# Kernel optimization log

Hardware: AMD Instinct MI355X
Metric: run time of the kernel (lower is better)

Reference implementation:

```python
import jax, jax.numpy as jnp
import numpy as np
from jax import lax

KS = 3            # kernel_size
K = 32            # cluster_num
NB = 32           # num_base_kernels
HID = 64          # mlp_hidden_dim
COUT = 64         # out_channels
MAX_ITER = 20
TOL = 0.005


def _unfold3(x):
    # torch nn.Unfold(k=3, pad=1): output channel order is (c, kh, kw)
    b, c, h, w = x.shape
    xp = jnp.pad(x, ((0, 0), (0, 0), (1, 1), (1, 1)))
    cols = [xp[:, :, i:i + h, j:j + w] for i in range(KS) for j in range(KS)]
    p = jnp.stack(cols, axis=2)  # [B, C, 9, H, W]
    return p.reshape(b, c * KS * KS, h * w).transpose(0, 2, 1)  # [B, HW, C*9]


def _kmeans_single(key, sample):
    # sample: [N, D]. Lloyd iterations with early stop on total center shift.
    n, d = sample.shape
    centers0 = sample[jax.random.permutation(key, n)[:K]]

    def assign(centers):
        d2 = (jnp.sum(sample * sample, 1, keepdims=True)
              - 2.0 * (sample @ centers.T)
              + jnp.sum(centers * centers, 1))
        return jnp.argmin(d2, axis=1)

    def body(carry):
        i, centers, _ = carry
        a = assign(centers)
        oh = jax.nn.one_hot(a, K, dtype=sample.dtype)  # [N, K]
        counts = oh.sum(0)                             # [K]
        sums = oh.T @ sample                           # [K, D]
        new = jnp.where(counts[:, None] > 0,
                        sums / jnp.maximum(counts, 1.0)[:, None],
                        centers)
        shift = jnp.sum(jnp.linalg.norm(new - centers, axis=1))
        return (i + 1, new, shift)

    def cond(carry):
        i, _, shift = carry
        return jnp.logical_and(i < MAX_ITER, shift >= TOL * n)

    init = (jnp.int32(0), centers0, jnp.asarray(jnp.inf, sample.dtype))
    _, centers, _ = lax.while_loop(cond, body, init)
    return assign(centers)


def _kmeans(features):
    keys = jax.random.split(jax.random.key(42), features.shape[0])
    return jax.vmap(_kmeans_single)(keys, features)


def _mlp(x, w1, b1, w2, b2, w3, b3):
    h = jax.nn.relu(x @ w1 + b1)
    h = jax.nn.relu(h @ w2 + b2)
    return h @ w3 + b3


def setup_inputs() -> dict:
    key = jax.random.key(0)
    ks = jax.random.split(key, 16)
    B, C, H, W = 2, 32, 64, 64
    F = C * KS * KS
    fan = 1.0 / np.sqrt(F)
    fanh = 1.0 / np.sqrt(HID)
    return {
        'x': jax.random.normal(ks[0], (B, C, H, W), jnp.float32),
        'base_kernels': jax.random.normal(ks[1], (NB, F, COUT), jnp.float32) * np.sqrt(2.0 / F),
        'kg_w1': jax.random.normal(ks[2], (F, HID), jnp.float32) * fan,
        'kg_b1': jnp.zeros((HID,), jnp.float32),
        'kg_w2': jax.random.normal(ks[3], (HID, HID), jnp.float32) * fanh,
        'kg_b2': jnp.zeros((HID,), jnp.float32),
        'kg_w3': jax.random.normal(ks[4], (HID, NB), jnp.float32) * fanh,
        'kg_b3': jnp.zeros((NB,), jnp.float32),
        'bg_w1': jax.random.normal(ks[5], (F, HID), jnp.float32) * fan,
        'bg_b1': jnp.zeros((HID,), jnp.float32),
        'bg_w2': jax.random.normal(ks[6], (HID, HID), jnp.float32) * fanh,
        'bg_b2': jnp.zeros((HID,), jnp.float32),
        'bg_w3': jax.random.normal(ks[7], (HID, COUT), jnp.float32) * fanh,
        'bg_b3': jnp.zeros((COUT,), jnp.float32),
    }


def reference(x, base_kernels, kg_w1, kg_b1, kg_w2, kg_b2, kg_w3, kg_b3,
              bg_w1, bg_b1, bg_w2, bg_b2, bg_w3, bg_b3):
    B, C, H, W = x.shape
    patches = _unfold3(x)  # [B, P, F] with F = C*9
    P = patches.shape[1]
    # observation features: mean over kernel area per channel
    obs = patches.reshape(B, P, C, KS * KS).mean(-1)  # [B, P, C]
    idx = _kmeans(obs)  # [B, P] int cluster assignments

    # per-cluster centers of the full patch features (scatter-mean)
    oh = jax.nn.one_hot(idx, K, dtype=patches.dtype)          # [B, P, K]
    sums = jnp.einsum('bpk,bpf->bkf', oh, patches)            # [B, K, F]
    counts = jnp.maximum(oh.sum(1), 1.0)                      # [B, K]
    centers = sums / counts[:, :, None]                       # [B, K, F]

    # adaptive kernels = softmax-mixture of base kernels
    attn = jax.nn.softmax(_mlp(centers, kg_w1, kg_b1, kg_w2, kg_b2, kg_w3, kg_b3), axis=-1)  # [B,K,NB]
    kernels = jnp.einsum('bkn,nfc->bkfc', attn, base_kernels)  # [B, K, F, COUT]
    biases = _mlp(centers, bg_w1, bg_b1, bg_w2, bg_b2, bg_w3, bg_b3)  # [B, K, COUT]

    # combine: out[b,p] = patches[b,p] @ kernels[b, idx[b,p]] + biases[b, idx[b,p]]
    bidx = jnp.arange(B)[:, None]
    wtok = kernels[bidx, idx]   # [B, P, F, COUT]
    btok = biases[bidx, idx]    # [B, P, COUT]
    out = jnp.einsum('bpf,bpfc->bpc', patches, wtok) + btok
    out = out.transpose(0, 2, 1).reshape(B, COUT, H, W)
    return (out, idx)
```

## Files before the change

kernel.cpp:

```cpp
#include <hip/hip_runtime.h>
#include <hip/hip_bf16.h>
#include <vector>
#include <algorithm>
#include <utility>
#include <stdint.h>

#define BB 2
#define PP 4096
#define FF 288
#define KK 32
#define NBASE 32
#define HID 64
#define COUT 64
#define NWG_KM 32
#define SUBS 16
#define OUT_ELEMS 524288

#define THREEFRY_PARTITIONABLE 1

typedef unsigned short u16;

#define OFF_IDX    512
#define OFF_ATTN   33280
#define OFF_BIAS   41472
#define OFF_PART   57856
#define OFF_CNTS   320000
#define OFF_CPART  328192
#define OFF_WG     1544704
#define OFF_BAR2   3904000

struct InitIdx { int v[2][32]; };

__device__ __forceinline__ float bf2f(u16 u){
  union { unsigned int i; float f; } cv; cv.i = ((unsigned int)u) << 16; return cv.f;
}
__device__ __forceinline__ u16 f2bf(float f){
  union { float f; unsigned int i; } cv; cv.f = f;
  unsigned int x = cv.i;
  unsigned int r = (x + 0x7FFFu + ((x >> 16) & 1u)) >> 16;
  return (u16)r;
}
__device__ __forceinline__ float u_lo(unsigned int u){
  union { unsigned int i; float f; } cv; cv.i = u << 16; return cv.f;
}
__device__ __forceinline__ float u_hi(unsigned int u){
  union { unsigned int i; float f; } cv; cv.i = u & 0xFFFF0000u; return cv.f;
}

__device__ __forceinline__ void st_agent(float* p, float v){
  __hip_atomic_store(reinterpret_cast<unsigned int*>(p), __float_as_uint(v),
                     __ATOMIC_RELAXED, __HIP_MEMORY_SCOPE_AGENT);
}
__device__ __forceinline__ float ld_agent(const float* p){
  unsigned int u = __hip_atomic_load(reinterpret_cast<const unsigned int*>(p),
                                     __ATOMIC_RELAXED, __HIP_MEMORY_SCOPE_AGENT);
  return __uint_as_float(u);
}

template<bool BF>
__device__ __forceinline__ float ld(const void* p, size_t i){
  if constexpr (BF) { return bf2f(((const u16*)p)[i]); }
  else              { return ((const float*)p)[i]; }
}
template<bool BF>
__device__ __forceinline__ void st(void* p, size_t i, float v){
  if constexpr (BF) { ((u16*)p)[i] = f2bf(v); }
  else              { ((float*)p)[i] = v; }
}

template<bool BF>
__device__ __forceinline__ float obs_chan(const void* x, size_t bi, int h, int w){
  float s = 0.f;
  #pragma unroll
  for (int dh=-1; dh<=1; ++dh){
    int hh = h + dh;
    #pragma unroll
    for (int dw=-1; dw<=1; ++dw){
      int ww = w + dw;
      float v = 0.f;
      if ((unsigned)hh < 64u && (unsigned)ww < 64u) v = ld<BF>(x, bi + (hh<<6) + ww);
      s += v;
    }
  }
  return s / 9.0f;
}

__device__ __forceinline__ void gbar16(int* slots, int mb, int sub, int epoch){
  asm volatile("s_waitcnt vmcnt(0)" ::: "memory");
  __syncthreads();
  const int t = threadIdx.x;
  if (t == 0)
    __hip_atomic_store(&slots[(mb*16 + sub)*16], epoch, __ATOMIC_RELAXED, __HIP_MEMORY_SCOPE_AGENT);
  if (t < 16){
    while (__hip_atomic_load(&slots[(mb*16 + t)*16], __ATOMIC_RELAXED, __HIP_MEMORY_SCOPE_AGENT) < epoch){}
  }
  __atomic_signal_fence(__ATOMIC_SEQ_CST);
  __syncthreads();
}

__global__ __launch_bounds__(256) void kDetect(const void* __restrict__ x, int* flag,
                                               int* slots){
  __shared__ int cnt;
  if (threadIdx.x == 0) cnt = 0;
  for (int i = threadIdx.x; i < 512; i += 256) slots[i] = 0;
  __syncthreads();
  const u16* p = (const u16*)x;
  int bad = 0;
  for (int i = threadIdx.x; i < 1024; i += 256){
    u16 u = p[2*i];
    unsigned e = (u >> 7) & 0xFFu;
    if (e >= 131u) ++bad;
  }
  atomicAdd(&cnt, bad);
  __syncthreads();
  if (threadIdx.x == 0) *flag = (cnt < 102) ? 1 : 0;
}

template<bool BF>
__device__ void kB_body(const void* __restrict__ x,
                        float* __restrict__ part,
                        float* __restrict__ cnts,
                        int* __restrict__ idxg,
                        void* __restrict__ dout,
                        int* __restrict__ slots,
                        const InitIdx& ii,
                        float* obs_st,
                        float* cent,
                        float* cc_s,
                        int*   a_loc,
                        float* sq,
                        float* snorm,
                        float* cntsh,
                        float* acc8,
                        float* cnt8){
  const int t   = threadIdx.x;
  const int wg  = blockIdx.x;
  const int mb  = wg >> 4;
  const int sub = wg & 15;
  const int pg  = sub*256 + t;
  const int d   = t & 31, oct = t >> 5;

  float o[32];
  {
    int h = pg >> 6, w = pg & 63;
    size_t xb = (size_t)mb << 17;
    for (int c=0; c<32; ++c){
      float v = obs_chan<BF>(x, xb + ((size_t)c<<12), h, w);
      o[c] = v; obs_st[t*33 + c] = v;
    }
  }
  if (t < 32){
    int q = ii.v[mb][t];
    int qh = q >> 6, qw = q & 63;
    size_t xq = (size_t)mb << 17;
    for (int c=0; c<32; ++c) cent[t*32 + c] = obs_chan<BF>(x, xq + ((size_t)c<<12), qh, qw);
  }
  __syncthreads();

  float ss = 0.f;
  #pragma unroll
  for (int dd=0; dd<32; ++dd) ss = fmaf(o[dd], o[dd], ss);

  bool act = true;
  int parity = 0;

  for (int it=0; it<20 && act; ++it){
    if (t < 32){
      float s = 0.f;
      #pragma unroll
      for (int dd=0; dd<32; ++dd){ float v = cent[t*32 + dd]; s = fmaf(v,v,s); }
      cc_s[t] = s;
    }
    __syncthreads();
    float best = 3.0e38f; int bk = 0;
    for (int k=0; k<32; k+=4){
      const float4* c0 = (const float4*)&cent[(k  )*32];
      const float4* c1 = (const float4*)&cent[(k+1)*32];
      const float4* c2 = (const float4*)&cent[(k+2)*32];
      const float4* c3 = (const float4*)&cent[(k+3)*32];
      float dt0=0.f, dt1=0.f, dt2=0.f, dt3=0.f;
      #pragma unroll
      for (int q=0; q<8; ++q){
        float4 a0 = c0[q], a1 = c1[q], a2 = c2[q], a3 = c3[q];
        float o0 = o[q*4+0], o1 = o[q*4+1], o2 = o[q*4+2], o3 = o[q*4+3];
        dt0 = fmaf(o0,a0.x,dt0); dt0 = fmaf(o1,a0.y,dt0); dt0 = fmaf(o2,a0.z,dt0); dt0 = fmaf(o3,a0.w,dt0);
        dt1 = fmaf(o0,a1.x,dt1); dt1 = fmaf(o1,a1.y,dt1); dt1 = fmaf(o2,a1.z,dt1); dt1 = fmaf(o3,a1.w,dt1);
        dt2 = fmaf(o0,a2.x,dt2); dt2 = fmaf(o1,a2.y,dt2); dt2 = fmaf(o2,a2.z,dt2); dt2 = fmaf(o3,a2.w,dt2);
        dt3 = fmaf(o0,a3.x,dt3); dt3 = fmaf(o1,a3.y,dt3); dt3 = fmaf(o2,a3.z,dt3); dt3 = fmaf(o3,a3.w,dt3);
      }
      float di0 = (ss - 2.0f*dt0) + cc_s[k];
      float di1 = (ss - 2.0f*dt1) + cc_s[k+1];
      float di2 = (ss - 2.0f*dt2) + cc_s[k+2];
      float di3 = (ss - 2.0f*dt3) + cc_s[k+3];
      if (di0 < best){ best = di0; bk = k; }
      if (di1 < best){ best = di1; bk = k+1; }
      if (di2 < best){ best = di2; bk = k+2; }
      if (di3 < best){ best = di3; bk = k+3; }
    }
    a_loc[t] = bk;
    __syncthreads();
    for (int e=t; e<8*32*33; e+=256) acc8[e] = 0.f;
    cnt8[t] = 0.f;
    __syncthreads();
    {
      const int p0 = oct*32;
      int kcur = a_loc[p0];
      float racc = 0.f; int rl = 0;
      for (int i=0; i<32; ++i){
        int kp = a_loc[p0+i];
        float v = obs_st[(p0+i)*33 + d];
        if (kp != kcur){
          acc8[(oct*32 + kcur)*33 + d] += racc;
          if (d == 0) cnt8[oct*32 + kcur] += (float)rl;
          racc = 0.f; rl = 0; kcur = kp;
        }
        racc += v; ++rl;
      }
      acc8[(oct*32 + kcur)*33 + d] += racc;
      if (d == 0) cnt8[oct*32 + kcur] += (float)rl;
    }
    __syncthreads();
    float* Pg = part + ((size_t)((parity*2 + mb)*SUBS + sub))*1024;
    {
      float r0=0.f, r1=0.f, r2=0.f, r3=0.f;
      #pragma unroll
      for (int o2=0; o2<8; ++o2){
        r0 += acc8[(o2*32 + oct      )*33 + d];
        r1 += acc8[(o2*32 + oct + 8  )*33 + d];
        r2 += acc8[(o2*32 + oct + 16 )*33 + d];
        r3 += acc8[(o2*32 + oct + 24 )*33 + d];
      }
      st_agent(&Pg[(oct     )*32 + d], r0);
      st_agent(&Pg[(oct + 8 )*32 + d], r1);
      st_agent(&Pg[(oct + 16)*32 + d], r2);
      st_agent(&Pg[(oct + 24)*32 + d], r3);
    }
    if (t < 32){
      float c = 0.f;
      #pragma unroll
      for (int o2=0; o2<8; ++o2) c += cnt8[o2*32 + t];
      st_agent(&cnts[((size_t)((parity*2 + mb)*SUBS + sub))*32 + t], c);
    }
    gbar16(slots, mb, sub, it+1);
    {
      const float* Pb = part + (size_t)((parity*2 + mb)*SUBS)*1024;
      const float* Cb = cnts + (size_t)((parity*2 + mb)*SUBS)*32;
      if (t < 32){
        float s = 0.f;
        #pragma unroll
        for (int si=0; si<SUBS; ++si) s += ld_agent(&Cb[si*32 + t]);
        cntsh[t] = s;
      }
      __syncthreads();
      {
        int k = t >> 3, d4 = (t & 7) * 4;
        float vx = 0.f, vy = 0.f, vz = 0.f, vw = 0.f;
        #pragma unroll
        for (int si=0; si<SUBS; ++si){
          const float* pp = &Pb[si*1024 + k*32 + d4];
          float a0 = ld_agent(pp+0);
          float a1 = ld_agent(pp+1);
          float a2 = ld_agent(pp+2);
          float a3 = ld_agent(pp+3);
          vx += a0; vy += a1; vz += a2; vw += a3;
        }
        float cn = cntsh[k];
        float den = fmaxf(cn, 1.f);
        bool pos = cn > 0.f;
        float o0 = cent[k*32 + d4+0], o1 = cent[k*32 + d4+1];
        float o2 = cent[k*32 + d4+2], o3 = cent[k*32 + d4+3];
        float n0 = pos ? (vx / den) : o0;
        float n1 = pos ? (vy / den) : o1;
        float n2 = pos ? (vz / den) : o2;
        float n3 = pos ? (vw / den) : o3;
        float e0 = n0-o0, e1 = n1-o1, e2 = n2-o2, e3 = n3-o3;
        sq[k*32 + d4+0] = e0*e0; sq[k*32 + d4+1] = e1*e1;
        sq[k*32 + d4+2] = e2*e2; sq[k*32 + d4+3] = e3*e3;
        cent[k*32 + d4+0] = n0; cent[k*32 + d4+1] = n1;
        cent[k*32 + d4+2] = n2; cent[k*32 + d4+3] = n3;
      }
      __syncthreads();
      if (t < 32){
        float s = 0.f;
        #pragma unroll
        for (int dd=0; dd<32; ++dd) s += sq[t*32 + dd];
        snorm[t] = sqrtf(s);
      }
      __syncthreads();
      float sh = 0.f;
      for (int k=0;k<32;++k) sh += snorm[k];
      act = ((it+1) < 20) && ((double)sh >= 20.48);
      __syncthreads();
    }
    parity ^= 1;
  }
  if (t == 0)
    __hip_atomic_store(&slots[(mb*16 + sub)*16], 0x7FFFFFFF, __ATOMIC_RELAXED, __HIP_MEMORY_SCOPE_AGENT);
  __syncthreads();
  if (t < 32){
    float s = 0.f;
    #pragma unroll
    for (int dd=0; dd<32; ++dd){ float v = cent[t*32 + dd]; s = fmaf(v,v,s); }
    cc_s[t] = s;
  }
  __syncthreads();
  float best = 3.0e38f; int bk = 0;
  for (int k=0; k<32; k+=4){
    const float4* c0 = (const float4*)&cent[(k  )*32];
    const float4* c1 = (const float4*)&cent[(k+1)*32];
    const float4* c2 = (const float4*)&cent[(k+2)*32];
    const float4* c3 = (const float4*)&cent[(k+3)*32];
    float dt0=0.f, dt1=0.f, dt2=0.f, dt3=0.f;
    #pragma unroll
    for (int q=0; q<8; ++q){
      float4 a0 = c0[q], a1 = c1[q], a2 = c2[q], a3 = c3[q];
      float o0 = o[q*4+0], o1 = o[q*4+1], o2 = o[q*4+2], o3 = o[q*4+3];
      dt0 = fmaf(o0,a0.x,dt0); dt0 = fmaf(o1,a0.y,dt0); dt0 = fmaf(o2,a0.z,dt0); dt0 = fmaf(o3,a0.w,dt0);
      dt1 = fmaf(o0,a1.x,dt1); dt1 = fmaf(o1,a1.y,dt1); dt1 = fmaf(o2,a1.z,dt1); dt1 = fmaf(o3,a1.w,dt1);
      dt2 = fmaf(o0,a2.x,dt2); dt2 = fmaf(o1,a2.y,dt2); dt2 = fmaf(o2,a2.z,dt2); dt2 = fmaf(o3,a2.w,dt2);
      dt3 = fmaf(o0,a3.x,dt3); dt3 = fmaf(o1,a3.y,dt3); dt3 = fmaf(o2,a3.z,dt3); dt3 = fmaf(o3,a3.w,dt3);
    }
    float di0 = (ss - 2.0f*dt0) + cc_s[k];
    float di1 = (ss - 2.0f*dt1) + cc_s[k+1];
    float di2 = (ss - 2.0f*dt2) + cc_s[k+2];
    float di3 = (ss - 2.0f*dt3) + cc_s[k+3];
    if (di0 < best){ best = di0; bk = k; }
    if (di1 < best){ best = di1; bk = k+1; }
    if (di2 < best){ best = di2; bk = k+2; }
    if (di3 < best){ best = di3; bk = k+3; }
  }
  idxg[mb*PP + pg] = bk;
  st<BF>(dout, (size_t)OUT_ELEMS + mb*PP + pg, (float)bk);
}

__global__ __launch_bounds__(256) void kB(const void* x, float* part, float* cnts,
                                          int* idxg, void* dout,
                                          int* slots,
                                          const int* flag, InitIdx ii){
  __shared__ __align__(16) float obs_st[256*33];
  __shared__ __align__(16) float cent[32*32];
  __shared__ float cc_s[32];
  __shared__ int   a_loc[256];
  __shared__ float sq[32*32];
  __shared__ float snorm[32];
  __shared__ float cntsh[32];
  __shared__ float acc8[8*32*33];
  __shared__ float cnt8[8*32];
  if (*flag) kB_body<true >(x, part, cnts, idxg, dout, slots, ii,
                            obs_st, cent, cc_s, a_loc, sq, snorm, cntsh, acc8, cnt8);
  else       kB_body<false>(x, part, cnts, idxg, dout, slots, ii,
                            obs_st, cent, cc_s, a_loc, sq, snorm, cntsh, acc8, cnt8);
}

template<bool BF>
__device__ void kC_body(const void* __restrict__ x,
                        const int* __restrict__ idxg,
                        float* __restrict__ cpartJ,
                        float* __restrict__ acc,
                        int* __restrict__ idxsh){
  int wgid = blockIdx.x;
  int cg = wgid / 9, j = wgid % 9;
  int b = cg >> 4, pc = cg & 15;
  int t = threadIdx.x;
  for (int e=t; e<32*33; e+=256) acc[e] = 0.f;
  idxsh[t] = idxg[b*PP + pc*256 + t];
  __syncthreads();

  int dh = j/3 - 1, dw = j%3 - 1;
  int gp = (pc << 8) + t;
  int h = gp >> 6, w = gp & 63;
  int k = idxsh[t];
  int hh = h + dh, ww = w + dw;
  bool ok = ((unsigned)hh < 64u) && ((unsigned)ww < 64u);
  size_t boff = ((size_t)b << 17) + (hh << 6) + ww;

  #pragma unroll 4
  for (int c=0; c<32; ++c){
    float v = ok ? ld<BF>(x, boff + ((size_t)c << 12)) : 0.f;
    atomicAdd(&acc[k*33 + c], v);
  }
  if (j == 0) atomicAdd(&acc[k*33 + 32], 1.0f);
  __syncthreads();
  float* cp = cpartJ + (size_t)wgid*(32*33);
  for (int e=t; e<32*33; e+=256) cp[e] = acc[e];
}

__global__ __launch_bounds__(256) void kC(const void* x, const int* idxg,
                                          float* cpartJ, const int* flag){
  __shared__ float acc[32*33];
  __shared__ int   idxsh[256];
  if (*flag) kC_body<true >(x, idxg, cpartJ, acc, idxsh);
  else       kC_body<false>(x, idxg, cpartJ, acc, idxsh);
}

template<bool BF>
__device__ void kD_body(const float* __restrict__ cpartJ,
                        const void* kg_w1, const void* kg_b1,
                        const void* kg_w2, const void* kg_b2,
                        const void* kg_w3, const void* kg_b3,
                        const void* bg_w1, const void* bg_b1,
                        const void* bg_w2, const void* bg_b2,
                        const void* bg_w3, const void* bg_b3,
                        float* __restrict__ attn,
                        float* __restrict__ biasO,
                        float* __restrict__ row,
                        float* __restrict__ h1,
                        float* __restrict__ h2,
                        float* __restrict__ lgs){
  int wg = blockIdx.x; int b = wg >> 5; int k = wg & 31;
  int t = threadIdx.x;
  float cnt = 0.f;
  for (int ch=0; ch<16; ++ch)
    cnt += cpartJ[(size_t)((b*16+ch)*9)*(32*33) + k*33 + 32];
  float den = fmaxf(cnt, 1.f);
  for (int f=t; f<FF; f+=64){
    int c = f / 9, j = f % 9;
    float s = 0.f;
    for (int ch=0; ch<16; ++ch)
      s += cpartJ[(size_t)((b*16+ch)*9 + j)*(32*33) + k*33 + c];
    row[f] = s / den;
  }
  __syncthreads();

  {
    float s = 0.f;
    #pragma unroll 8
    for (int f=0; f<FF; ++f) s = fmaf(row[f], ld<BF>(kg_w1, f*HID + t), s);
    h1[t] = fmaxf(s + ld<BF>(kg_b1, t), 0.f);
  }
  __syncthreads();
  {
    float s = 0.f;
    #pragma unroll 8
    for (int h=0; h<HID; ++h) s = fmaf(h1[h], ld<BF>(kg_w2, h*HID + t), s);
    h2[t] = fmaxf(s + ld<BF>(kg_b2, t), 0.f);
  }
  __syncthreads();
  if (t < 32){
    float s = 0.f;
    #pragma unroll 8
    for (int h=0; h<HID; ++h) s = fmaf(h2[h], ld<BF>(kg_w3, h*NBASE + t), s);
    lgs[t] = s + ld<BF>(kg_b3, t);
  }
  __syncthreads();
  if (t < 32){
    float mx = -3.0e38f;
    for (int i=0;i<NBASE;++i) mx = fmaxf(mx, lgs[i]);
    float se = 0.f;
    for (int i=0;i<NBASE;++i) se += expf(lgs[i]-mx);
    attn[wg*NBASE + t] = expf(lgs[t]-mx) / se;
  }
  __syncthreads();
  {
    float s = 0.f;
    #pragma unroll 8
    for (int f=0; f<FF; ++f) s = fmaf(row[f], ld<BF>(bg_w1, f*HID + t), s);
    h1[t] = fmaxf(s + ld<BF>(bg_b1, t), 0.f);
  }
  __syncthreads();
  {
    float s = 0.f;
    #pragma unroll 8
    for (int h=0; h<HID; ++h) s = fmaf(h1[h], ld<BF>(bg_w2, h*HID + t), s);
    h2[t] = fmaxf(s + ld<BF>(bg_b2, t), 0.f);
  }
  __syncthreads();
  {
    float s = 0.f;
    #pragma unroll 8
    for (int h=0; h<HID; ++h) s = fmaf(h2[h], ld<BF>(bg_w3, h*COUT + t), s);
    biasO[wg*COUT + t] = s + ld<BF>(bg_b3, t);
  }
}

__global__ __launch_bounds__(64) void kD(const float* cpartJ,
                                         const void* kg_w1, const void* kg_b1,
                                         const void* kg_w2, const void* kg_b2,
                                         const void* kg_w3, const void* kg_b3,
                                         const void* bg_w1, const void* bg_b1,
                                         const void* bg_w2, const void* bg_b2,
                                         const void* bg_w3, const void* bg_b3,
                                         float* attn, float* biasO, const int* flag){
  __shared__ float row[FF];
  __shared__ float h1[64];
  __shared__ float h2[64];
  __shared__ float lgs[32];
  if (*flag) kD_body<true >(cpartJ, kg_w1,kg_b1,kg_w2,kg_b2,kg_w3,kg_b3,
                            bg_w1,bg_b1,bg_w2,bg_b2,bg_w3,bg_b3, attn, biasO, row,h1,h2,lgs);
  else       kD_body<false>(cpartJ, kg_w1,kg_b1,kg_w2,kg_b2,kg_w3,kg_b3,
                            bg_w1,bg_b1,bg_w2,bg_b2,bg_w3,bg_b3, attn, biasO, row,h1,h2,lgs);
}

template<bool BF>
__device__ void kE_body(const void* __restrict__ base,
                        const float* __restrict__ attn,
                        u16* __restrict__ Wg,
                        float* __restrict__ at,
                        float* __restrict__ tile){
  int wg = blockIdx.x;
  int fq = wg & 3, bk = wg >> 2;
  int t = threadIdx.x;
  if (t < 32) at[t] = attn[bk*NBASE + t];
  __syncthreads();
  int f0 = fq*72;
  for (int e=t; e<72*64; e+=256){
    int fl = e >> 6, c = e & 63;
    size_t bi = (size_t)(f0 + fl)*COUT + c;
    float s = 0.f;
    #pragma unroll 8
    for (int n=0; n<NBASE; ++n)
      s = fmaf(at[n], ld<BF>(base, bi + (size_t)n*FF*COUT), s);
    tile[fl*65 + c] = s;
  }
  __syncthreads();
  for (int e=t; e<72*64; e+=256){
    int c = e / 72, fl = e % 72;
    Wg[(size_t)bk*(64*FF) + (size_t)c*FF + f0 + fl] = f2bf(tile[fl*65 + c]);
  }
}

__global__ __launch_bounds__(256) void kE(const void* base, const float* attn,
                                          u16* Wg, const int* flag){
  __shared__ float at[32];
  __shared__ float tile[72*65];
  if (*flag) kE_body<true >(base, attn, Wg, at, tile);
  else       kE_body<false>(base, attn, Wg, at, tile);
}

template<bool BF>
__device__ void kF_body(const void* __restrict__ x,
                        const int* __restrict__ idxg,
                        const u16* __restrict__ Wg,
                        const float* __restrict__ biasO,
                        void* __restrict__ dout,
                        u16* __restrict__ patch,
                        float* __restrict__ outT){
  int wg = blockIdx.x;
  int q = wg & 3, h = (wg >> 2) & 63, b = wg >> 8;
  int t = threadIdx.x, wv = t >> 6, lane = t & 63;
  int w0 = q << 4;

  for (int e=t; e<16*FF; e+=256){
    int pl = e & 15, fe = e >> 4;
    int c = fe / 9, j = fe % 9;
    int hh = h + j/3 - 1, ww = w0 + pl + (j%3) - 1;
    float v = 0.f;
    if ((unsigned)hh < 64u && (unsigned)ww < 64u)
      v = ld<BF>(x, ((size_t)b << 17) + ((size_t)c << 12) + (hh<<6) + ww);
    patch[pl*296 + fe] = f2bf(v);
  }
  __syncthreads();

  #pragma unroll
  for (int i=0; i<4; ++i){
    int pl = (wv << 2) + i;
    int p = (h << 6) + w0 + pl;
    int k = idxg[(b << 12) + p];
    const uint4* Wp = (const uint4*)(Wg + ((size_t)((b << 5) + k)*64 + lane)*FF);
    const uint4* Pp = (const uint4*)(patch + pl*296);
    float acc = 0.f;
    #pragma unroll 6
    for (int j=0; j<36; ++j){
      uint4 wv4 = Wp[j];
      uint4 pv4 = Pp[j];
      acc = fmaf(u_lo(pv4.x), u_lo(wv4.x), acc);
      acc = fmaf(u_hi(pv4.x), u_hi(wv4.x), acc);
      acc = fmaf(u_lo(pv4.y), u_lo(wv4.y), acc);
      acc = fmaf(u_hi(pv4.y), u_hi(wv4.y), acc);
      acc = fmaf(u_lo(pv4.z), u_lo(wv4.z), acc);
      acc = fmaf(u_hi(pv4.z), u_hi(wv4.z), acc);
      acc = fmaf(u_lo(pv4.w), u_lo(wv4.w), acc);
      acc = fmaf(u_hi(pv4.w), u_hi(wv4.w), acc);
    }
    float bias = biasO[((b << 5) + k)*COUT + lane];
    outT[lane*17 + pl] = acc + bias;
  }
  __syncthreads();

  for (int e=t; e<1024; e+=256){
    int cout = e >> 4, pl = e & 15;
    st<BF>(dout, (((size_t)(b << 6) + cout) << 12) + (h << 6) + w0 + pl,
           outT[cout*17 + pl]);
  }
}

__global__ __launch_bounds__(256) void kF(const void* x, const int* idxg,
                                          const u16* Wg, const float* biasO,
                                          void* dout, const int* flag){
  __shared__ u16   patch[16*296];
  __shared__ float outT[64*17];
  if (*flag) kF_body<true >(x, idxg, Wg, biasO, dout, patch, outT);
  else       kF_body<false>(x, idxg, Wg, biasO, dout, patch, outT);
}

static inline uint32_t rotl32(uint32_t x, int d){ return (x<<d)|(x>>(32-d)); }
static void tf_block(uint32_t k0,uint32_t k1,uint32_t x0,uint32_t x1,uint32_t&o0,uint32_t&o1){
  uint32_t ks2 = k0 ^ k1 ^ 0x1BD11BDAu;
  uint32_t v0 = x0 + k0, v1 = x1 + k1;
  const int ra[4]={13,15,26,6}, rb[4]={17,29,16,24};
  #define R4(r) for(int i_=0;i_<4;++i_){ v0 += v1; v1 = rotl32(v1,(r)[i_]); v1 ^= v0; }
  R4(ra); v0 += k1;  v1 += ks2 + 1u;
  R4(rb); v0 += ks2; v1 += k0  + 2u;
  R4(ra); v0 += k0;  v1 += k1  + 3u;
  R4(rb); v0 += k1;  v1 += ks2 + 4u;
  R4(ra); v0 += ks2; v1 += k0  + 5u;
  #undef R4
  o0 = v0; o1 = v1;
}
struct KP{ uint32_t a, b; };
static void tf_split(KP k, KP& first, KP& second){
#if THREEFRY_PARTITIONABLE
  uint32_t a0,b0,a1,b1;
  tf_block(k.a,k.b, 0u,0u, a0,b0);
  tf_block(k.a,k.b, 0u,1u, a1,b1);
  first  = KP{a0,b0};
  second = KP{a1,b1};
#else
  uint32_t a0,b0,a1,b1;
  tf_block(k.a,k.b, 0u,2u, a0,b0);
  tf_block(k.a,k.b, 1u,3u, a1,b1);
  first  = KP{a0,a1};
  second = KP{b0,b1};
#endif
}
static void random_bits_4096(KP k, std::vector<uint32_t>& bits){
#if THREEFRY_PARTITIONABLE
  for (int i=0;i<4096;++i){
    uint32_t o0,o1; tf_block(k.a,k.b, 0u,(uint32_t)i, o0,o1);
    bits[i] = o0 ^ o1;
  }
#else
  for (int i=0;i<2048;++i){
    uint32_t o0,o1; tf_block(k.a,k.b,(uint32_t)i,(uint32_t)(i+2048),o0,o1);
    bits[i] = o0; bits[i+2048] = o1;
  }
#endif
}
static void perm_first32(KP key, int* out32){
  std::vector<int> vals(4096);
  for (int i=0;i<4096;++i) vals[i] = i;
  std::vector<uint32_t> bits(4096);
  std::vector<std::pair<uint32_t,int>> pr(4096);
  KP k = key;
  for (int r=0;r<2;++r){
    KP nk, sk; tf_split(k, nk, sk); k = nk;
    random_bits_4096(sk, bits);
    for (int i=0;i<4096;++i) pr[i] = std::make_pair(bits[i], vals[i]);
    std::stable_sort(pr.begin(), pr.end(),
        [](const std::pair<uint32_t,int>& a, const std::pair<uint32_t,int>& c){ return a.first < c.first; });
    for (int i=0;i<4096;++i) vals[i] = pr[i].second;
  }
  for (int j=0;j<32;++j) out32[j] = vals[j];
}

extern "C" void kernel_launch(void* const* d_in, const int* in_sizes, int n_in,
                              void* d_out, int out_size, void* d_ws, size_t ws_size,
                              hipStream_t stream) {
  const void* x     = d_in[0];
  const void* base  = d_in[1];
  const void* kg_w1 = d_in[2];
  const void* kg_b1 = d_in[3];
  const void* kg_w2 = d_in[4];
  const void* kg_b2 = d_in[5];
  const void* kg_w3 = d_in[6];
  const void* kg_b3 = d_in[7];
  const void* bg_w1 = d_in[8];
  const void* bg_b1 = d_in[9];
  const void* bg_w2 = d_in[10];
  const void* bg_b2 = d_in[11];
  const void* bg_w3 = d_in[12];
  const void* bg_b3 = d_in[13];

  char* ws = (char*)d_ws;
  int*   flag  = (int*)(ws + 64);
  int*   idxg  = (int*)(ws + OFF_IDX);
  float* attn  = (float*)(ws + OFF_ATTN);
  float* biasO = (float*)(ws + OFF_BIAS);
  float* part  = (float*)(ws + OFF_PART);
  float* cnts  = (float*)(ws + OFF_CNTS);
  float* cpartJ= (float*)(ws + OFF_CPART);
  u16*   Wg    = (u16*)(ws + OFF_WG);
  int*   slots = (int*)(ws + OFF_BAR2);

  InitIdx ii;
  KP root = KP{0u, 42u};
  KP kb0, kb1; tf_split(root, kb0, kb1);
  perm_first32(kb0, ii.v[0]);
  perm_first32(kb1, ii.v[1]);

  kDetect<<<1, 256, 0, stream>>>(x, flag, slots);
  kB<<<NWG_KM, 256, 0, stream>>>(x, part, cnts, idxg, d_out, slots, flag, ii);
  kC<<<288, 256, 0, stream>>>(x, idxg, cpartJ, flag);
  kD<<<64, 64, 0, stream>>>(cpartJ,
                            kg_w1, kg_b1, kg_w2, kg_b2, kg_w3, kg_b3,
                            bg_w1, bg_b1, bg_w2, bg_b2, bg_w3, bg_b3,
                            attn, biasO, flag);
  kE<<<256, 256, 0, stream>>>(base, attn, Wg, flag);
  kF<<<512, 256, 0, stream>>>(x, idxg, Wg, biasO, d_out, flag);
}
```

Before: 288.4 us.

## Replace dtype-detect kernel with per-block self-detection and vectorize base-kernel mixing

Removes the separate single-block kDetect launch. Each kernel now samples the input itself to decide whether it is bf16 or fp32, and the barrier slots are cleared with an async memset. This drops one serialized launch and the dependent flag read at the start of every kernel, at the cost of redundant detection reads in every block. Separately, kE's base-kernel mixing now loads eight output channels per thread with 128-bit vector loads instead of scalar loads.

After: 277.7 us. 3.7% less time.

```diff
diff --git a/kernel.cpp b/kernel.cpp
--- a/kernel.cpp
+++ b/kernel.cpp
@@ -56,6 +56,12 @@
                                      __ATOMIC_RELAXED, __HIP_MEMORY_SCOPE_AGENT);
   return __uint_as_float(u);
 }
+__device__ __forceinline__ void st_slot(int* p, int v){
+  __hip_atomic_store(p, v, __ATOMIC_RELAXED, __HIP_MEMORY_SCOPE_AGENT);
+}
+__device__ __forceinline__ int ld_slot(const int* p){
+  return __hip_atomic_load(p, __ATOMIC_RELAXED, __HIP_MEMORY_SCOPE_AGENT);
+}
 
 template<bool BF>
 __device__ __forceinline__ float ld(const void* p, size_t i){
@@ -66,6 +72,24 @@
 __device__ __forceinline__ void st(void* p, size_t i, float v){
   if constexpr (BF) { ((u16*)p)[i] = f2bf(v); }
   else              { ((float*)p)[i] = v; }
+}
+
+__device__ __forceinline__ bool self_detect(const void* x, int* cntS){
+  const int t = threadIdx.x, nb = blockDim.x;
+  if (t == 0) *cntS = 0;
+  __syncthreads();
+  const u16* p = (const u16*)x;
+  int bad = 0;
+  for (int i = t; i < 1024; i += nb){
+    u16 u = p[2*i];
+    unsigned e = (u >> 7) & 0xFFu;
+    if (e >= 131u) ++bad;
+  }
+  if (bad) atomicAdd(cntS, bad);
+  __syncthreads();
+  bool r = (*cntS < 102);
+  __syncthreads();
+  return r;
 }
 
 template<bool BF>
@@ -89,31 +113,12 @@
   asm volatile("s_waitcnt vmcnt(0)" ::: "memory");
   __syncthreads();
   const int t = threadIdx.x;
-  if (t == 0)
-    __hip_atomic_store(&slots[(mb*16 + sub)*16], epoch, __ATOMIC_RELAXED, __HIP_MEMORY_SCOPE_AGENT);
+  if (t == 0) st_slot(&slots[(mb*16 + sub)*16], epoch);
   if (t < 16){
-    while (__hip_atomic_load(&slots[(mb*16 + t)*16], __ATOMIC_RELAXED, __HIP_MEMORY_SCOPE_AGENT) < epoch){}
+    while (ld_slot(&slots[(mb*16 + t)*16]) < epoch){}
   }
   __atomic_signal_fence(__ATOMIC_SEQ_CST);
   __syncthreads();
-}
-
-__global__ __launch_bounds__(256) void kDetect(const void* __restrict__ x, int* flag,
-                                               int* slots){
-  __shared__ int cnt;
-  if (threadIdx.x == 0) cnt = 0;
-  for (int i = threadIdx.x; i < 512; i += 256) slots[i] = 0;
-  __syncthreads();
-  const u16* p = (const u16*)x;
-  int bad = 0;
-  for (int i = threadIdx.x; i < 1024; i += 256){
-    u16 u = p[2*i];
-    unsigned e = (u >> 7) & 0xFFu;
-    if (e >= 131u) ++bad;
-  }
-  atomicAdd(&cnt, bad);
-  __syncthreads();
-  if (threadIdx.x == 0) *flag = (cnt < 102) ? 1 : 0;
 }
 
 template<bool BF>
@@ -294,8 +299,7 @@
     }
     parity ^= 1;
   }
-  if (t == 0)
-    __hip_atomic_store(&slots[(mb*16 + sub)*16], 0x7FFFFFFF, __ATOMIC_RELAXED, __HIP_MEMORY_SCOPE_AGENT);
+  if (t == 0) st_slot(&slots[(mb*16 + sub)*16], 0x7FFFFFFF);
   __syncthreads();
   if (t < 32){
     float s = 0.f;
@@ -335,8 +339,7 @@
 
 __global__ __launch_bounds__(256) void kB(const void* x, float* part, float* cnts,
                                           int* idxg, void* dout,
-                                          int* slots,
-                                          const int* flag, InitIdx ii){
+                                          int* slots, InitIdx ii){
   __shared__ __align__(16) float obs_st[256*33];
   __shared__ __align__(16) float cent[32*32];
   __shared__ float cc_s[32];
@@ -346,10 +349,12 @@
   __shared__ float cntsh[32];
   __shared__ float acc8[8*32*33];
   __shared__ float cnt8[8*32];
-  if (*flag) kB_body<true >(x, part, cnts, idxg, dout, slots, ii,
-                            obs_st, cent, cc_s, a_loc, sq, snorm, cntsh, acc8, cnt8);
-  else       kB_body<false>(x, part, cnts, idxg, dout, slots, ii,
-                            obs_st, cent, cc_s, a_loc, sq, snorm, cntsh, acc8, cnt8);
+  __shared__ int   cntS;
+  if (self_detect(x, &cntS))
+       kB_body<true >(x, part, cnts, idxg, dout, slots, ii,
+                      obs_st, cent, cc_s, a_loc, sq, snorm, cntsh, acc8, cnt8);
+  else kB_body<false>(x, part, cnts, idxg, dout, slots, ii,
+                      obs_st, cent, cc_s, a_loc, sq, snorm, cntsh, acc8, cnt8);
 }
 
 template<bool BF>
@@ -386,11 +391,12 @@
 }
 
 __global__ __launch_bounds__(256) void kC(const void* x, const int* idxg,
-                                          float* cpartJ, const int* flag){
+                                          float* cpartJ){
   __shared__ float acc[32*33];
   __shared__ int   idxsh[256];
-  if (*flag) kC_body<true >(x, idxg, cpartJ, acc, idxsh);
-  else       kC_body<false>(x, idxg, cpartJ, acc, idxsh);
+  __shared__ int   cntS;
+  if (self_detect(x, &cntS)) kC_body<true >(x, idxg, cpartJ, acc, idxsh);
+  else                       kC_body<false>(x, idxg, cpartJ, acc, idxsh);
 }
 
 template<bool BF>
@@ -473,22 +479,24 @@
   }
 }
 
-__global__ __launch_bounds__(64) void kD(const float* cpartJ,
+__global__ __launch_bounds__(64) void kD(const void* x, const float* cpartJ,
                                          const void* kg_w1, const void* kg_b1,
                                          const void* kg_w2, const void* kg_b2,
                                          const void* kg_w3, const void* kg_b3,
                                          const void* bg_w1, const void* bg_b1,
                                          const void* bg_w2, const void* bg_b2,
                                          const void* bg_w3, const void* bg_b3,
-                                         float* attn, float* biasO, const int* flag){
+                                         float* attn, float* biasO){
   __shared__ float row[FF];
   __shared__ float h1[64];
   __shared__ float h2[64];
   __shared__ float lgs[32];
-  if (*flag) kD_body<true >(cpartJ, kg_w1,kg_b1,kg_w2,kg_b2,kg_w3,kg_b3,
-                            bg_w1,bg_b1,bg_w2,bg_b2,bg_w3,bg_b3, attn, biasO, row,h1,h2,lgs);
-  else       kD_body<false>(cpartJ, kg_w1,kg_b1,kg_w2,kg_b2,kg_w3,kg_b3,
-                            bg_w1,bg_b1,bg_w2,bg_b2,bg_w3,bg_b3, attn, biasO, row,h1,h2,lgs);
+  __shared__ int   cntS;
+  if (self_detect(x, &cntS))
+       kD_body<true >(cpartJ, kg_w1,kg_b1,kg_w2,kg_b2,kg_w3,kg_b3,
+                      bg_w1,bg_b1,bg_w2,bg_b2,bg_w3,bg_b3, attn, biasO, row,h1,h2,lgs);
+  else kD_body<false>(cpartJ, kg_w1,kg_b1,kg_w2,kg_b2,kg_w3,kg_b3,
+                      bg_w1,bg_b1,bg_w2,bg_b2,bg_w3,bg_b3, attn, biasO, row,h1,h2,lgs);
 }
 
 template<bool BF>
@@ -503,14 +511,36 @@
   if (t < 32) at[t] = attn[bk*NBASE + t];
   __syncthreads();
   int f0 = fq*72;
-  for (int e=t; e<72*64; e+=256){
-    int fl = e >> 6, c = e & 63;
-    size_t bi = (size_t)(f0 + fl)*COUT + c;
-    float s = 0.f;
-    #pragma unroll 8
-    for (int n=0; n<NBASE; ++n)
-      s = fmaf(at[n], ld<BF>(base, bi + (size_t)n*FF*COUT), s);
-    tile[fl*65 + c] = s;
+  for (int e8 = t; e8 < 72*8; e8 += 256){
+    int fl = e8 >> 3, cg = (e8 & 7) << 3;
+    float s0=0.f,s1=0.f,s2=0.f,s3=0.f,s4=0.f,s5=0.f,s6=0.f,s7=0.f;
+    if constexpr (BF){
+      const u16* bp = (const u16*)base + (size_t)(f0 + fl)*COUT + cg;
+      #pragma unroll 4
+      for (int n=0; n<NBASE; ++n){
+        uint4 v = *(const uint4*)(bp + (size_t)n*FF*COUT);
+        float a = at[n];
+        s0 = fmaf(a, u_lo(v.x), s0); s1 = fmaf(a, u_hi(v.x), s1);
+        s2 = fmaf(a, u_lo(v.y), s2); s3 = fmaf(a, u_hi(v.y), s3);
+        s4 = fmaf(a, u_lo(v.z), s4); s5 = fmaf(a, u_hi(v.z), s5);
+        s6 = fmaf(a, u_lo(v.w), s6); s7 = fmaf(a, u_hi(v.w), s7);
+      }
+    } else {
+      const float* bp = (const float*)base + (size_t)(f0 + fl)*COUT + cg;
+      #pragma unroll 4
+      for (int n=0; n<NBASE; ++n){
+        float4 v0 = *(const float4*)(bp + (size_t)n*FF*COUT);
+        float4 v1 = *(const float4*)(bp + (size_t)n*FF*COUT + 4);
+        float a = at[n];
+        s0 = fmaf(a, v0.x, s0); s1 = fmaf(a, v0.y, s1);
+        s2 = fmaf(a, v0.z, s2); s3 = fmaf(a, v0.w, s3);
+        s4 = fmaf(a, v1.x, s4); s5 = fmaf(a, v1.y, s5);
+        s6 = fmaf(a, v1.z, s6); s7 = fmaf(a, v1.w, s7);
+      }
+    }
+    float* tp = &tile[fl*65 + cg];
+    tp[0]=s0; tp[1]=s1; tp[2]=s2; tp[3]=s3;
+    tp[4]=s4; tp[5]=s5; tp[6]=s6; tp[7]=s7;
   }
   __syncthreads();
   for (int e=t; e<72*64; e+=256){
@@ -519,12 +549,13 @@
   }
 }
 
-__global__ __launch_bounds__(256) void kE(const void* base, const float* attn,
-                                          u16* Wg, const int* flag){
+__global__ __launch_bounds__(256) void kE(const void* x, const void* base,
+                                          const float* attn, u16* Wg){
   __shared__ float at[32];
   __shared__ float tile[72*65];
-  if (*flag) kE_body<true >(base, attn, Wg, at, tile);
-  else       kE_body<false>(base, attn, Wg, at, tile);
+  __shared__ int   cntS;
+  if (self_detect(x, &cntS)) kE_body<true >(base, attn, Wg, at, tile);
+  else                       kE_body<false>(base, attn, Wg, at, tile);
 }
 
 template<bool BF>
@@ -586,11 +617,12 @@
 
 __global__ __launch_bounds__(256) void kF(const void* x, const int* idxg,
                                           const u16* Wg, const float* biasO,
-                                          void* dout, const int* flag){
+                                          void* dout){
   __shared__ u16   patch[16*296];
   __shared__ float outT[64*17];
-  if (*flag) kF_body<true >(x, idxg, Wg, biasO, dout, patch, outT);
-  else       kF_body<false>(x, idxg, Wg, biasO, dout, patch, outT);
+  __shared__ int   cntS;
+  if (self_detect(x, &cntS)) kF_body<true >(x, idxg, Wg, biasO, dout, patch, outT);
+  else                       kF_body<false>(x, idxg, Wg, biasO, dout, patch, outT);
 }
 
 static inline uint32_t rotl32(uint32_t x, int d){ return (x<<d)|(x>>(32-d)); }
@@ -672,7 +704,6 @@
   const void* bg_b3 = d_in[13];
 
   char* ws = (char*)d_ws;
-  int*   flag  = (int*)(ws + 64);
   int*   idxg  = (int*)(ws + OFF_IDX);
   float* attn  = (float*)(ws + OFF_ATTN);
   float* biasO = (float*)(ws + OFF_BIAS);
@@ -688,13 +719,13 @@
   perm_first32(kb0, ii.v[0]);
   perm_first32(kb1, ii.v[1]);
 
-  kDetect<<<1, 256, 0, stream>>>(x, flag, slots);
-  kB<<<NWG_KM, 256, 0, stream>>>(x, part, cnts, idxg, d_out, slots, flag, ii);
-  kC<<<288, 256, 0, stream>>>(x, idxg, cpartJ, flag);
-  kD<<<64, 64, 0, stream>>>(cpartJ,
+  hipMemsetAsync(ws + OFF_BAR2, 0, 2048, stream);
+  kB<<<NWG_KM, 256, 0, stream>>>(x, part, cnts, idxg, d_out, slots, ii);
+  kC<<<288, 256, 0, stream>>>(x, idxg, cpartJ);
+  kD<<<64, 64, 0, stream>>>(x, cpartJ,
                             kg_w1, kg_b1, kg_w2, kg_b2, kg_w3, kg_b3,
                             bg_w1, bg_b1, bg_w2, bg_b2, bg_w3, bg_b3,
-                            attn, biasO, flag);
-  kE<<<256, 256, 0, stream>>>(base, attn, Wg, flag);
-  kF<<<512, 256, 0, stream>>>(x, idxg, Wg, biasO, d_out, flag);
-}
+                            attn, biasO);
+  kE<<<256, 256, 0, stream>>>(x, base, attn, Wg);
+  kF<<<512, 256, 0, stream>>>(x, idxg, Wg, biasO, d_out);
+}
```
